# Performance work log

Measured on AMD Instinct MI355X. Metric: run time of the kernel, lower is better.

Reference implementation:

```python
import jax, jax.numpy as jnp
import numpy as np

EMBED_DIM = 1024
NUM_HEADS = 16
HEAD_DIM = EMBED_DIM // NUM_HEADS


def setup_inputs() -> dict:
    key = jax.random.key(0)
    ks = jax.random.split(key, 9)
    B, S, D = 2, 2048, EMBED_DIM
    scale = 1.0 / np.sqrt(D)
    x = jax.random.normal(ks[0], (B, S, D), dtype=jnp.float32)
    Wq = jax.random.normal(ks[1], (D, D), dtype=jnp.float32) * scale
    Wk = jax.random.normal(ks[2], (D, D), dtype=jnp.float32) * scale
    Wv = jax.random.normal(ks[3], (D, D), dtype=jnp.float32) * scale
    Wo = jax.random.normal(ks[4], (D, D), dtype=jnp.float32) * scale
    bq = jnp.zeros((D,), jnp.float32)
    bk = jnp.zeros((D,), jnp.float32)
    bv = jnp.zeros((D,), jnp.float32)
    bo = jnp.zeros((D,), jnp.float32)
    return {"x": x, "Wq": Wq, "bq": bq, "Wk": Wk, "bk": bk,
            "Wv": Wv, "bv": bv, "Wo": Wo, "bo": bo}


def reference(x, Wq, bq, Wk, bk, Wv, bv, Wo, bo):
    B, S, D = x.shape
    H, Dh = NUM_HEADS, HEAD_DIM
    # QKV projections -> [B, H, S, Dh]
    q = (x @ Wq + bq).reshape(B, S, H, Dh).transpose(0, 2, 1, 3)
    k = (x @ Wk + bk).reshape(B, S, H, Dh).transpose(0, 2, 1, 3)
    v = (x @ Wv + bv).reshape(B, S, H, Dh).transpose(0, 2, 1, 3)
    # scores [B, H, S, S], scaled by sqrt(head_dim)
    scores = jnp.einsum('bhqd,bhkd->bhqk', q, k) / jnp.sqrt(jnp.float32(Dh))
    attn = jax.nn.softmax(scores, axis=-1)
    out = jnp.einsum('bhqk,bhkd->bhqd', attn, v)  # [B, H, S, Dh]
    out = out.transpose(0, 2, 1, 3).reshape(B, S, D)
    return out @ Wo + bo
```

## Files before the change

### kernel.cpp

```cpp
#include <hip/hip_runtime.h>
#include <hip/hip_bf16.h>

typedef short bf16x8 __attribute__((ext_vector_type(8)));
typedef float f32x4 __attribute__((ext_vector_type(4)));
typedef unsigned uint2v __attribute__((ext_vector_type(2)));

#define MFMA16(a, b, c) __builtin_amdgcn_mfma_f32_16x16x32_bf16((a), (b), (c), 0, 0, 0)

#if __has_builtin(__builtin_amdgcn_exp2f)
#define EXP2(x) __builtin_amdgcn_exp2f(x)
#else
#define EXP2(x) exp2f(x)
#endif

static constexpr int B_ = 2, S_ = 2048, D_ = 1024, H_ = 16, DH = 64;
static constexpr int M_ = B_ * S_;
static constexpr int K_ = D_;
static constexpr float kQS = 0.18033688011112042f;

static __device__ __forceinline__ ushort f2bf(float f) {
    __hip_bfloat16 h = __float2bfloat16(f);
    return *reinterpret_cast<ushort*>(&h);
}

static __device__ __forceinline__ void gload16(const ushort* g, ushort* l) {
    __builtin_amdgcn_global_load_lds((const __attribute__((address_space(1))) void*)g,
                                     (__attribute__((address_space(3))) void*)l, 16, 0, 0);
}

static __device__ __forceinline__ unsigned pkbf(float lo, float hi) {
    return __builtin_amdgcn_perm(__builtin_bit_cast(unsigned, hi),
                                 __builtin_bit_cast(unsigned, lo), 0x07060302u);
}

__global__ __launch_bounds__(256) void prep5(const float* __restrict__ x,
                                             const float* __restrict__ W0,
                                             const float* __restrict__ W1,
                                             const float* __restrict__ W2,
                                             const float* __restrict__ W3,
                                             ushort* __restrict__ xb,
                                             ushort* __restrict__ T0,
                                             ushort* __restrict__ T1,
                                             ushort* __restrict__ T2,
                                             ushort* __restrict__ T3) {
    int z = blockIdx.z;
    int tx = threadIdx.x, ty = threadIdx.y;
    int t = ty * 32 + tx;
    if (z == 4) {
        int blk = blockIdx.y * 32 + blockIdx.x;
#pragma unroll
        for (int k = 0; k < 4; k++) {
            int i = blk * 1024 + k * 256 + t;
            float4 v = reinterpret_cast<const float4*>(x)[i];
            ushort4 o;
            o.x = f2bf(v.x); o.y = f2bf(v.y); o.z = f2bf(v.z); o.w = f2bf(v.w);
            reinterpret_cast<ushort4*>(xb)[i] = o;
        }
        return;
    }
    __shared__ float tile[32][33];
    const float* W = (z == 0) ? W0 : (z == 1) ? W1 : (z == 2) ? W2 : W3;
    ushort* T = (z == 0) ? T0 : (z == 1) ? T1 : (z == 2) ? T2 : T3;
    float sc = (z == 0) ? kQS : 1.0f;
    int bx = blockIdx.x, by = blockIdx.y;
#pragma unroll
    for (int i = 0; i < 4; i++)
        tile[ty + i * 8][tx] = W[(by * 32 + ty + i * 8) * D_ + bx * 32 + tx];
    __syncthreads();
#pragma unroll
    for (int i = 0; i < 4; i++)
        T[(bx * 32 + ty + i * 8) * K_ + by * 32 + tx] = f2bf(tile[tx][ty + i * 8] * sc);
}

template <int MODE, int TN>
__global__ __launch_bounds__(256, 3) void gemm128(const ushort* __restrict__ A,
                                                  const ushort* __restrict__ Wt,
                                                  const float* __restrict__ bias_q,
                                                  const float* __restrict__ bias_k,
                                                  const float* __restrict__ bias_v,
                                                  ushort* __restrict__ Qb,
                                                  ushort* __restrict__ Kb,
                                                  ushort* __restrict__ Vtb,
                                                  float* __restrict__ outf) {
    constexpr int NJ = TN / 32;
    __shared__ __align__(16) ushort As[128 * 32];
    __shared__ __align__(16) ushort Bs[TN * 32];

    int m0 = blockIdx.x * 128;
    int n0 = blockIdx.y * TN;
    int t = threadIdx.x;
    int lane = t & 63, w = t >> 6;
    int ln = lane & 15, lq = lane >> 4;
    int wm = (w >> 1) * 64, wn = (w & 1) * (TN / 2);

    int c0 = t, c1 = t + 256;
    const ushort* Ag0 = A + (size_t)(m0 + (c0 >> 2)) * K_ + (c0 & 3) * 8;
    const ushort* Ag1 = A + (size_t)(m0 + (c1 >> 2)) * K_ + (c1 & 3) * 8;
    const ushort* Bg0 = Wt + (size_t)(n0 + (c0 >> 2)) * K_ + (c0 & 3) * 8;
    const ushort* Bg1 = Wt + (size_t)(n0 + (c1 >> 2)) * K_ + (c1 & 3) * 8;
    ushort* Al0 = As + c0 * 8;
    ushort* Al1 = As + c1 * 8;
    ushort* Bl0 = Bs + c0 * 8;
    ushort* Bl1 = Bs + c1 * 8;

    const bool swp = (MODE == 1) || (n0 < 2048);

    f32x4 acc[4][NJ];
#pragma unroll
    for (int i = 0; i < 4; i++)
#pragma unroll
        for (int j = 0; j < NJ; j++) acc[i][j] = f32x4{0.f, 0.f, 0.f, 0.f};

    if (swp) {
        for (int k0 = 0; k0 < K_; k0 += 32) {
            gload16(Ag0 + k0, Al0);
            gload16(Ag1 + k0, Al1);
            gload16(Bg0 + k0, Bl0);
            if (TN == 128) gload16(Bg1 + k0, Bl1);
            __syncthreads();
            bf16x8 af[4], bfr[NJ];
#pragma unroll
            for (int i = 0; i < 4; i++)
                af[i] = *reinterpret_cast<const bf16x8*>(As + (wm + i * 16 + ln) * 32 + lq * 8);
#pragma unroll
            for (int j = 0; j < NJ; j++)
                bfr[j] = *reinterpret_cast<const bf16x8*>(Bs + (wn + j * 16 + ln) * 32 + lq * 8);
#pragma unroll
            for (int i = 0; i < 4; i++)
#pragma unroll
                for (int j = 0; j < NJ; j++)
                    acc[i][j] = MFMA16(bfr[j], af[i], acc[i][j]);
            __syncthreads();
        }
    } else {
        for (int k0 = 0; k0 < K_; k0 += 32) {
            gload16(Ag0 + k0, Al0);
            gload16(Ag1 + k0, Al1);
            gload16(Bg0 + k0, Bl0);
            if (TN == 128) gload16(Bg1 + k0, Bl1);
            __syncthreads();
            bf16x8 af[4], bfr[NJ];
#pragma unroll
            for (int i = 0; i < 4; i++)
                af[i] = *reinterpret_cast<const bf16x8*>(As + (wm + i * 16 + ln) * 32 + lq * 8);
#pragma unroll
            for (int j = 0; j < NJ; j++)
                bfr[j] = *reinterpret_cast<const bf16x8*>(Bs + (wn + j * 16 + ln) * 32 + lq * 8);
#pragma unroll
            for (int i = 0; i < 4; i++)
#pragma unroll
                for (int j = 0; j < NJ; j++)
                    acc[i][j] = MFMA16(af[i], bfr[j], acc[i][j]);
            __syncthreads();
        }
    }

    if (MODE == 1) {
#pragma unroll
        for (int j = 0; j < NJ; j++) {
            int nb = n0 + wn + j * 16 + lq * 4;
            float4 bv4 = *reinterpret_cast<const float4*>(bias_q + nb);
#pragma unroll
            for (int i = 0; i < 4; i++) {
                int m = m0 + wm + i * 16 + ln;
                float4 o;
                o.x = acc[i][j][0] + bv4.x;
                o.y = acc[i][j][1] + bv4.y;
                o.z = acc[i][j][2] + bv4.z;
                o.w = acc[i][j][3] + bv4.w;
                *reinterpret_cast<float4*>(outf + (size_t)m * D_ + nb) = o;
            }
        }
    } else if (n0 < 2048) {
        int which = n0 >> 10;
        const float* bp = which ? bias_k : bias_q;
        ushort* dst = which ? Kb : Qb;
        float bsc = which ? 1.0f : kQS;
#pragma unroll
        for (int j = 0; j < NJ; j++) {
            int nb = ((n0 + wn + j * 16) & 1023) + lq * 4;
            int h = nb >> 6, dhb = nb & 63;
            float4 bv4 = *reinterpret_cast<const float4*>(bp + nb);
            bv4.x *= bsc; bv4.y *= bsc; bv4.z *= bsc; bv4.w *= bsc;
#pragma unroll
            for (int i = 0; i < 4; i++) {
                int m = m0 + wm + i * 16 + ln;
                int b = m >> 11, s = m & 2047;
                ushort4 o4;
                o4.x = f2bf(acc[i][j][0] + bv4.x);
                o4.y = f2bf(acc[i][j][1] + bv4.y);
                o4.z = f2bf(acc[i][j][2] + bv4.z);
                o4.w = f2bf(acc[i][j][3] + bv4.w);
                *reinterpret_cast<ushort4*>(dst + (((size_t)(b * H_ + h) * S_) + s) * DH + dhb) = o4;
            }
        }
    } else {
#pragma unroll
        for (int j = 0; j < NJ; j++) {
            int n = n0 + wn + j * 16 + ln;
            int nn = n & 1023, h = nn >> 6, dh = nn & 63;
            float bv = bias_v[nn];
#pragma unroll
            for (int i = 0; i < 4; i++) {
                int m = m0 + wm + i * 16 + lq * 4;
                int b = m >> 11, s0 = m & 2047;
                ushort4 o4;
                o4.x = f2bf(acc[i][j][0] + bv);
                o4.y = f2bf(acc[i][j][1] + bv);
                o4.z = f2bf(acc[i][j][2] + bv);
                o4.w = f2bf(acc[i][j][3] + bv);
                *reinterpret_cast<ushort4*>(Vtb + (((size_t)(b * H_ + h) * DH) + dh) * S_ + s0) = o4;
            }
        }
    }
}

__global__ __launch_bounds__(256) void attn64t(const ushort* __restrict__ Q,
                                               const ushort* __restrict__ K,
                                               const ushort* __restrict__ Vt,
                                               ushort* __restrict__ O) {
    __shared__ __align__(16) ushort Kl[512 * 8];
    __shared__ __align__(16) ushort Vl[512 * 8];
    __shared__ __align__(16) ushort Pl[4][16 * 72];

    int bid = blockIdx.x;
    int qb = bid & 31;
    int bh = bid >> 5;
    int t = threadIdx.x;
    int lane = t & 63, w = t >> 6;
    int ln = lane & 15, lq = lane >> 4;
    int qt = qb * 4 + w;

    const ushort* Qp = Q + (size_t)bh * S_ * DH;
    const ushort* Kp = K + (size_t)bh * S_ * DH;
    const ushort* Vp = Vt + (size_t)bh * DH * S_;

    bf16x8 qf0 = *reinterpret_cast<const bf16x8*>(Qp + (qt * 16 + ln) * DH + lq * 8);
    bf16x8 qf1 = *reinterpret_cast<const bf16x8*>(Qp + (qt * 16 + ln) * DH + 32 + lq * 8);

    bf16x8 ones;
#pragma unroll
    for (int j = 0; j < 8; j++) ones[j] = (short)0x3F80;

    int c0 = t, c1 = t + 256;
    const ushort* Kg0 = Kp + (size_t)(c0 & 63) * DH + (c0 >> 6) * 8;
    const ushort* Kg1 = Kp + (size_t)(c1 & 63) * DH + (c1 >> 6) * 8;
    const ushort* Vg0 = Vp + (size_t)(c0 & 63) * S_ + (c0 >> 6) * 8;
    const ushort* Vg1 = Vp + (size_t)(c1 & 63) * S_ + (c1 >> 6) * 8;
    ushort* Kl0 = Kl + c0 * 8;
    ushort* Kl1 = Kl + c1 * 8;
    ushort* Vl0 = Vl + c0 * 8;
    ushort* Vl1 = Vl + c1 * 8;

    f32x4 o_acc[4];
    f32x4 l_acc = {0.f, 0.f, 0.f, 0.f};
#pragma unroll
    for (int nt = 0; nt < 4; nt++) o_acc[nt] = f32x4{0.f, 0.f, 0.f, 0.f};

    for (int kt = 0; kt < S_ / 64; kt++) {
        int kb = kt * 64;
        gload16(Kg0 + (size_t)kb * DH, Kl0);
        gload16(Kg1 + (size_t)kb * DH, Kl1);
        gload16(Vg0 + kb, Vl0);
        gload16(Vg1 + kb, Vl1);
        __syncthreads();

        f32x4 sc[4];
#pragma unroll
        for (int nt = 0; nt < 4; nt++) {
            bf16x8 kf0 = *reinterpret_cast<const bf16x8*>(Kl + (lq * 64 + nt * 16 + ln) * 8);
            bf16x8 kf1 = *reinterpret_cast<const bf16x8*>(Kl + ((4 + lq) * 64 + nt * 16 + ln) * 8);
            f32x4 c = {0.f, 0.f, 0.f, 0.f};
            c = MFMA16(kf0, qf0, c);
            c = MFMA16(kf1, qf1, c);
            sc[nt] = c;
        }
#pragma unroll
        for (int nt = 0; nt < 4; nt++) {
            float p0 = EXP2(sc[nt][0]);
            float p1 = EXP2(sc[nt][1]);
            float p2 = EXP2(sc[nt][2]);
            float p3 = EXP2(sc[nt][3]);
            uint2v pk;
            pk.x = pkbf(p0, p1);
            pk.y = pkbf(p2, p3);
            *reinterpret_cast<uint2v*>(&Pl[w][ln * 72 + nt * 16 + lq * 4]) = pk;
        }
        bf16x8 pf0 = *reinterpret_cast<const bf16x8*>(&Pl[w][ln * 72 + lq * 8]);
        bf16x8 pf1 = *reinterpret_cast<const bf16x8*>(&Pl[w][ln * 72 + 32 + lq * 8]);
        l_acc = MFMA16(pf0, ones, l_acc);
        l_acc = MFMA16(pf1, ones, l_acc);
#pragma unroll
        for (int nt = 0; nt < 4; nt++) {
            bf16x8 vf0 = *reinterpret_cast<const bf16x8*>(Vl + (lq * 64 + nt * 16 + ln) * 8);
            bf16x8 vf1 = *reinterpret_cast<const bf16x8*>(Vl + ((4 + lq) * 64 + nt * 16 + ln) * 8);
            o_acc[nt] = MFMA16(pf0, vf0, o_acc[nt]);
            o_acc[nt] = MFMA16(pf1, vf1, o_acc[nt]);
        }
        __syncthreads();
    }

    float linv[4];
#pragma unroll
    for (int r = 0; r < 4; r++) linv[r] = 1.0f / l_acc[r];
    int b = bh >> 4, h = bh & 15;
#pragma unroll
    for (int nt = 0; nt < 4; nt++)
#pragma unroll
        for (int r = 0; r < 4; r++) {
            int s = qt * 16 + lq * 4 + r;
            O[((b * S_ + s) * H_ + h) * DH + nt * 16 + ln] =
                f2bf(o_acc[nt][r] * linv[r]);
        }
}

extern "C" void kernel_launch(void* const* d_in, const int* in_sizes, int n_in,
                              void* d_out, int out_size, void* d_ws, size_t ws_size,
                              hipStream_t stream) {
    const float* x  = (const float*)d_in[0];
    const float* Wq = (const float*)d_in[1];
    const float* bq = (const float*)d_in[2];
    const float* Wk = (const float*)d_in[3];
    const float* bk = (const float*)d_in[4];
    const float* Wv = (const float*)d_in[5];
    const float* bv = (const float*)d_in[6];
    const float* Wo = (const float*)d_in[7];
    const float* bo = (const float*)d_in[8];
    float* out = (float*)d_out;

    char* ws = (char*)d_ws;
    const size_t MB = 1024 * 1024;
    ushort* wtq = (ushort*)(ws + 0 * MB);
    ushort* wtk = (ushort*)(ws + 2 * MB);
    ushort* wtv = (ushort*)(ws + 4 * MB);
    ushort* wto = (ushort*)(ws + 6 * MB);
    ushort* xb  = (ushort*)(ws + 8 * MB);
    ushort* Qb  = (ushort*)(ws + 16 * MB);
    ushort* Kb  = (ushort*)(ws + 24 * MB);
    ushort* Vtb = (ushort*)(ws + 32 * MB);
    ushort* AO  = (ushort*)(ws + 40 * MB);

    prep5<<<dim3(32, 32, 5), dim3(32, 8), 0, stream>>>(
        x, Wq, Wk, Wv, Wo, xb, wtq, wtk, wtv, wto);

    gemm128<0, 128><<<dim3(M_ / 128, 3072 / 128), 256, 0, stream>>>(
        xb, wtq, bq, bk, bv, Qb, Kb, Vtb, nullptr);

    attn64t<<<32 * 32, 256, 0, stream>>>(Qb, Kb, Vtb, AO);

    gemm128<1, 64><<<dim3(M_ / 128, D_ / 64), 256, 0, stream>>>(
        AO, wto, bo, nullptr, nullptr, nullptr, nullptr, nullptr, out);
}
```

Measured before the change: 207.1 us.

## Split attention keys in two halves with 32-row query tiles per wave and combine

The attention kernel now gives each wave two 16-row query tiles, so every K/V tile loaded into LDS feeds twice as many MFMAs. The key dimension is split into two halves across blocks, keeping the grid at 1024 blocks. Each half writes a normalized partial output plus its softmax row sums, and a new combine kernel merges them by weighted sum. This adds an extra kernel, extra global traffic for the partial outputs, and a second bf16 rounding step in exchange for better K/V reuse.

```diff
diff --git a/kernel.cpp b/kernel.cpp
--- a/kernel.cpp
+++ b/kernel.cpp
@@ -21,6 +21,11 @@
 static __device__ __forceinline__ ushort f2bf(float f) {
     __hip_bfloat16 h = __float2bfloat16(f);
     return *reinterpret_cast<ushort*>(&h);
+}
+static __device__ __forceinline__ float bf2f(ushort u) {
+    __hip_bfloat16 h;
+    *reinterpret_cast<ushort*>(&h) = u;
+    return __bfloat162float(h);
 }
 
 static __device__ __forceinline__ void gload16(const ushort* g, ushort* l) {
@@ -215,28 +220,37 @@
     }
 }
 
-__global__ __launch_bounds__(256) void attn64t(const ushort* __restrict__ Q,
-                                               const ushort* __restrict__ K,
-                                               const ushort* __restrict__ Vt,
-                                               ushort* __restrict__ O) {
+__global__ __launch_bounds__(256, 4) void attn128s(const ushort* __restrict__ Q,
+                                                   const ushort* __restrict__ K,
+                                                   const ushort* __restrict__ Vt,
+                                                   ushort* __restrict__ O1,
+                                                   ushort* __restrict__ O2,
+                                                   float* __restrict__ L) {
     __shared__ __align__(16) ushort Kl[512 * 8];
     __shared__ __align__(16) ushort Vl[512 * 8];
-    __shared__ __align__(16) ushort Pl[4][16 * 72];
+    __shared__ __align__(16) ushort Pl[4][2][16 * 72];
 
     int bid = blockIdx.x;
-    int qb = bid & 31;
-    int bh = bid >> 5;
+    int half = bid >> 9;
+    int rem = bid & 511;
+    int qb = rem & 15;
+    int bh = rem >> 4;
     int t = threadIdx.x;
     int lane = t & 63, w = t >> 6;
     int ln = lane & 15, lq = lane >> 4;
-    int qt = qb * 4 + w;
+    int q0 = qb * 128 + w * 32;
 
     const ushort* Qp = Q + (size_t)bh * S_ * DH;
-    const ushort* Kp = K + (size_t)bh * S_ * DH;
-    const ushort* Vp = Vt + (size_t)bh * DH * S_;
-
-    bf16x8 qf0 = *reinterpret_cast<const bf16x8*>(Qp + (qt * 16 + ln) * DH + lq * 8);
-    bf16x8 qf1 = *reinterpret_cast<const bf16x8*>(Qp + (qt * 16 + ln) * DH + 32 + lq * 8);
+    const ushort* Kp = K + (size_t)bh * S_ * DH + (size_t)half * 1024 * DH;
+    const ushort* Vp = Vt + (size_t)bh * DH * S_ + (size_t)half * 1024;
+
+    bf16x8 qf[2][2];
+#pragma unroll
+    for (int tl = 0; tl < 2; tl++) {
+        const ushort* qp = Qp + (q0 + tl * 16 + ln) * DH + lq * 8;
+        qf[tl][0] = *reinterpret_cast<const bf16x8*>(qp);
+        qf[tl][1] = *reinterpret_cast<const bf16x8*>(qp + 32);
+    }
 
     bf16x8 ones;
 #pragma unroll
@@ -252,12 +266,16 @@
     ushort* Vl0 = Vl + c0 * 8;
     ushort* Vl1 = Vl + c1 * 8;
 
-    f32x4 o_acc[4];
-    f32x4 l_acc = {0.f, 0.f, 0.f, 0.f};
-#pragma unroll
-    for (int nt = 0; nt < 4; nt++) o_acc[nt] = f32x4{0.f, 0.f, 0.f, 0.f};
-
-    for (int kt = 0; kt < S_ / 64; kt++) {
+    f32x4 o_acc[2][4];
+    f32x4 l_acc[2];
+#pragma unroll
+    for (int tl = 0; tl < 2; tl++) {
+        l_acc[tl] = f32x4{0.f, 0.f, 0.f, 0.f};
+#pragma unroll
+        for (int nt = 0; nt < 4; nt++) o_acc[tl][nt] = f32x4{0.f, 0.f, 0.f, 0.f};
+    }
+
+    for (int kt = 0; kt < 16; kt++) {
         int kb = kt * 64;
         gload16(Kg0 + (size_t)kb * DH, Kl0);
         gload16(Kg1 + (size_t)kb * DH, Kl1);
@@ -265,53 +283,105 @@
         gload16(Vg1 + kb, Vl1);
         __syncthreads();
 
-        f32x4 sc[4];
+        f32x4 sc[2][4];
 #pragma unroll
         for (int nt = 0; nt < 4; nt++) {
             bf16x8 kf0 = *reinterpret_cast<const bf16x8*>(Kl + (lq * 64 + nt * 16 + ln) * 8);
             bf16x8 kf1 = *reinterpret_cast<const bf16x8*>(Kl + ((4 + lq) * 64 + nt * 16 + ln) * 8);
-            f32x4 c = {0.f, 0.f, 0.f, 0.f};
-            c = MFMA16(kf0, qf0, c);
-            c = MFMA16(kf1, qf1, c);
-            sc[nt] = c;
-        }
-#pragma unroll
-        for (int nt = 0; nt < 4; nt++) {
-            float p0 = EXP2(sc[nt][0]);
-            float p1 = EXP2(sc[nt][1]);
-            float p2 = EXP2(sc[nt][2]);
-            float p3 = EXP2(sc[nt][3]);
-            uint2v pk;
-            pk.x = pkbf(p0, p1);
-            pk.y = pkbf(p2, p3);
-            *reinterpret_cast<uint2v*>(&Pl[w][ln * 72 + nt * 16 + lq * 4]) = pk;
-        }
-        bf16x8 pf0 = *reinterpret_cast<const bf16x8*>(&Pl[w][ln * 72 + lq * 8]);
-        bf16x8 pf1 = *reinterpret_cast<const bf16x8*>(&Pl[w][ln * 72 + 32 + lq * 8]);
-        l_acc = MFMA16(pf0, ones, l_acc);
-        l_acc = MFMA16(pf1, ones, l_acc);
+#pragma unroll
+            for (int tl = 0; tl < 2; tl++) {
+                f32x4 c = {0.f, 0.f, 0.f, 0.f};
+                c = MFMA16(kf0, qf[tl][0], c);
+                c = MFMA16(kf1, qf[tl][1], c);
+                sc[tl][nt] = c;
+            }
+        }
+#pragma unroll
+        for (int tl = 0; tl < 2; tl++)
+#pragma unroll
+            for (int nt = 0; nt < 4; nt++) {
+                float p0 = EXP2(sc[tl][nt][0]);
+                float p1 = EXP2(sc[tl][nt][1]);
+                float p2 = EXP2(sc[tl][nt][2]);
+                float p3 = EXP2(sc[tl][nt][3]);
+                uint2v pk;
+                pk.x = pkbf(p0, p1);
+                pk.y = pkbf(p2, p3);
+                *reinterpret_cast<uint2v*>(&Pl[w][tl][ln * 72 + nt * 16 + lq * 4]) = pk;
+            }
+        bf16x8 pf[2][2];
+#pragma unroll
+        for (int tl = 0; tl < 2; tl++) {
+            pf[tl][0] = *reinterpret_cast<const bf16x8*>(&Pl[w][tl][ln * 72 + lq * 8]);
+            pf[tl][1] = *reinterpret_cast<const bf16x8*>(&Pl[w][tl][ln * 72 + 32 + lq * 8]);
+            l_acc[tl] = MFMA16(pf[tl][0], ones, l_acc[tl]);
+            l_acc[tl] = MFMA16(pf[tl][1], ones, l_acc[tl]);
+        }
 #pragma unroll
         for (int nt = 0; nt < 4; nt++) {
             bf16x8 vf0 = *reinterpret_cast<const bf16x8*>(Vl + (lq * 64 + nt * 16 + ln) * 8);
             bf16x8 vf1 = *reinterpret_cast<const bf16x8*>(Vl + ((4 + lq) * 64 + nt * 16 + ln) * 8);
-            o_acc[nt] = MFMA16(pf0, vf0, o_acc[nt]);
-            o_acc[nt] = MFMA16(pf1, vf1, o_acc[nt]);
+#pragma unroll
+            for (int tl = 0; tl < 2; tl++) {
+                o_acc[tl][nt] = MFMA16(pf[tl][0], vf0, o_acc[tl][nt]);
+                o_acc[tl][nt] = MFMA16(pf[tl][1], vf1, o_acc[tl][nt]);
+            }
         }
         __syncthreads();
     }
 
-    float linv[4];
-#pragma unroll
-    for (int r = 0; r < 4; r++) linv[r] = 1.0f / l_acc[r];
+    ushort* Op = half ? O2 : O1;
+    float* Lp = L + ((size_t)half * 32 + bh) * S_;
     int b = bh >> 4, h = bh & 15;
 #pragma unroll
-    for (int nt = 0; nt < 4; nt++)
+    for (int tl = 0; tl < 2; tl++) {
+        float linv[4];
 #pragma unroll
         for (int r = 0; r < 4; r++) {
-            int s = qt * 16 + lq * 4 + r;
-            O[((b * S_ + s) * H_ + h) * DH + nt * 16 + ln] =
-                f2bf(o_acc[nt][r] * linv[r]);
-        }
+            linv[r] = 1.0f / l_acc[tl][r];
+            if (ln == 0) Lp[q0 + tl * 16 + lq * 4 + r] = l_acc[tl][r];
+        }
+#pragma unroll
+        for (int nt = 0; nt < 4; nt++)
+#pragma unroll
+            for (int r = 0; r < 4; r++) {
+                int s = q0 + tl * 16 + lq * 4 + r;
+                Op[((b * S_ + s) * H_ + h) * DH + nt * 16 + ln] =
+                    f2bf(o_acc[tl][nt][r] * linv[r]);
+            }
+    }
+}
+
+__global__ __launch_bounds__(256) void attn_comb(const ushort* __restrict__ O1,
+                                                 const ushort* __restrict__ O2,
+                                                 const float* __restrict__ L,
+                                                 ushort* __restrict__ AO) {
+    int i = blockIdx.x * 256 + threadIdx.x;
+    int row = i >> 7;
+    int col = (i & 127) * 8;
+    int h = col >> 6;
+    int b = row >> 11, s = row & 2047;
+    int bh = b * 16 + h;
+    float l1 = L[(size_t)bh * S_ + s];
+    float l2 = L[((size_t)32 + bh) * S_ + s];
+    float inv = 1.0f / (l1 + l2);
+    float w1 = l1 * inv, w2 = l2 * inv;
+    size_t off = (size_t)row * D_ + col;
+    ushort4 a0 = reinterpret_cast<const ushort4*>(O1 + off)[0];
+    ushort4 a1 = reinterpret_cast<const ushort4*>(O1 + off)[1];
+    ushort4 b0 = reinterpret_cast<const ushort4*>(O2 + off)[0];
+    ushort4 b1 = reinterpret_cast<const ushort4*>(O2 + off)[1];
+    ushort4 o0, o1v;
+    o0.x = f2bf(w1 * bf2f(a0.x) + w2 * bf2f(b0.x));
+    o0.y = f2bf(w1 * bf2f(a0.y) + w2 * bf2f(b0.y));
+    o0.z = f2bf(w1 * bf2f(a0.z) + w2 * bf2f(b0.z));
+    o0.w = f2bf(w1 * bf2f(a0.w) + w2 * bf2f(b0.w));
+    o1v.x = f2bf(w1 * bf2f(a1.x) + w2 * bf2f(b1.x));
+    o1v.y = f2bf(w1 * bf2f(a1.y) + w2 * bf2f(b1.y));
+    o1v.z = f2bf(w1 * bf2f(a1.z) + w2 * bf2f(b1.z));
+    o1v.w = f2bf(w1 * bf2f(a1.w) + w2 * bf2f(b1.w));
+    reinterpret_cast<ushort4*>(AO + off)[0] = o0;
+    reinterpret_cast<ushort4*>(AO + off)[1] = o1v;
 }
 
 extern "C" void kernel_launch(void* const* d_in, const int* in_sizes, int n_in,
@@ -339,6 +409,9 @@
     ushort* Kb  = (ushort*)(ws + 24 * MB);
     ushort* Vtb = (ushort*)(ws + 32 * MB);
     ushort* AO  = (ushort*)(ws + 40 * MB);
+    ushort* O1  = (ushort*)(ws + 8 * MB);
+    ushort* O2  = (ushort*)(ws + 48 * MB);
+    float*  Lw  = (float*)(ws + 56 * MB);
 
     prep5<<<dim3(32, 32, 5), dim3(32, 8), 0, stream>>>(
         x, Wq, Wk, Wv, Wo, xb, wtq, wtk, wtv, wto);
@@ -346,7 +419,8 @@
     gemm128<0, 128><<<dim3(M_ / 128, 3072 / 128), 256, 0, stream>>>(
         xb, wtq, bq, bk, bv, Qb, Kb, Vtb, nullptr);
 
-    attn64t<<<32 * 32, 256, 0, stream>>>(Qb, Kb, Vtb, AO);
+    attn128s<<<1024, 256, 0, stream>>>(Qb, Kb, Vtb, O1, O2, Lw);
+    attn_comb<<<(M_ * D_ / 8) / 256, 256, 0, stream>>>(O1, O2, Lw, AO);
 
     gemm128<1, 64><<<dim3(M_ / 128, D_ / 64), 256, 0, stream>>>(
         AO, wto, bo, nullptr, nullptr, nullptr, nullptr, nullptr, out);
```

New measurement: 198.8 us. 4.0% less time.

## Split attention key tiles across waves with cross-wave output reduction

Applied to the files above, without the earlier changes.

Each wave now handles a 16-key slice of every 64-key tile for all 64 queries of the block, instead of one 16-query tile against all keys. The S^T result is reused directly as the B operand of a 16x16x16 MFMA for PV, which removes the LDS round trip for P and the ones-MFMA used for the row sum. Row sums are accumulated in registers with shuffles. Partial outputs are then reduced across waves through LDS at the end. In exchange the kernel uses more accumulator registers (64 floats of o_acc), issues more MFMAs at half K-depth, and adds an epilogue reduction with extra barriers.

```diff
diff --git a/kernel.cpp b/kernel.cpp
--- a/kernel.cpp
+++ b/kernel.cpp
@@ -2,10 +2,17 @@
 #include <hip/hip_bf16.h>
 
 typedef short bf16x8 __attribute__((ext_vector_type(8)));
+typedef short bf16x4 __attribute__((ext_vector_type(4)));
 typedef float f32x4 __attribute__((ext_vector_type(4)));
 typedef unsigned uint2v __attribute__((ext_vector_type(2)));
 
 #define MFMA16(a, b, c) __builtin_amdgcn_mfma_f32_16x16x32_bf16((a), (b), (c), 0, 0, 0)
+
+#if __has_builtin(__builtin_amdgcn_mfma_f32_16x16x16_bf16)
+#define MFMAK16(a, b, c) __builtin_amdgcn_mfma_f32_16x16x16_bf16((a), (b), (c), 0, 0, 0)
+#else
+#define MFMAK16(a, b, c) __builtin_amdgcn_mfma_f32_16x16x16bf16_1k((a), (b), (c), 0, 0, 0)
+#endif
 
 #if __has_builtin(__builtin_amdgcn_exp2f)
 #define EXP2(x) __builtin_amdgcn_exp2f(x)
@@ -215,13 +222,15 @@
     }
 }
 
-__global__ __launch_bounds__(256) void attn64t(const ushort* __restrict__ Q,
+__global__ __launch_bounds__(256) void attn_ks(const ushort* __restrict__ Q,
                                                const ushort* __restrict__ K,
                                                const ushort* __restrict__ Vt,
                                                ushort* __restrict__ O) {
-    __shared__ __align__(16) ushort Kl[512 * 8];
-    __shared__ __align__(16) ushort Vl[512 * 8];
-    __shared__ __align__(16) ushort Pl[4][16 * 72];
+    __shared__ __align__(16) ushort SM[8192 + 512];
+    ushort* Kl = SM;
+    ushort* Vl = SM + 4096;
+    float* Ored = (float*)SM;
+    float* lw = (float*)(SM + 8192);
 
     int bid = blockIdx.x;
     int qb = bid & 31;
@@ -229,18 +238,19 @@
     int t = threadIdx.x;
     int lane = t & 63, w = t >> 6;
     int ln = lane & 15, lq = lane >> 4;
-    int qt = qb * 4 + w;
+    int q0 = qb * 64;
 
     const ushort* Qp = Q + (size_t)bh * S_ * DH;
     const ushort* Kp = K + (size_t)bh * S_ * DH;
     const ushort* Vp = Vt + (size_t)bh * DH * S_;
 
-    bf16x8 qf0 = *reinterpret_cast<const bf16x8*>(Qp + (qt * 16 + ln) * DH + lq * 8);
-    bf16x8 qf1 = *reinterpret_cast<const bf16x8*>(Qp + (qt * 16 + ln) * DH + 32 + lq * 8);
-
-    bf16x8 ones;
-#pragma unroll
-    for (int j = 0; j < 8; j++) ones[j] = (short)0x3F80;
+    bf16x8 qf[4][2];
+#pragma unroll
+    for (int qt = 0; qt < 4; qt++) {
+        const ushort* qp = Qp + (q0 + qt * 16 + ln) * DH + lq * 8;
+        qf[qt][0] = *reinterpret_cast<const bf16x8*>(qp);
+        qf[qt][1] = *reinterpret_cast<const bf16x8*>(qp + 32);
+    }
 
     int c0 = t, c1 = t + 256;
     const ushort* Kg0 = Kp + (size_t)(c0 & 63) * DH + (c0 >> 6) * 8;
@@ -252,10 +262,12 @@
     ushort* Vl0 = Vl + c0 * 8;
     ushort* Vl1 = Vl + c1 * 8;
 
-    f32x4 o_acc[4];
-    f32x4 l_acc = {0.f, 0.f, 0.f, 0.f};
-#pragma unroll
-    for (int nt = 0; nt < 4; nt++) o_acc[nt] = f32x4{0.f, 0.f, 0.f, 0.f};
+    f32x4 o_acc[4][4];
+    float l_part[4] = {0.f, 0.f, 0.f, 0.f};
+#pragma unroll
+    for (int nt = 0; nt < 4; nt++)
+#pragma unroll
+        for (int qt = 0; qt < 4; qt++) o_acc[nt][qt] = f32x4{0.f, 0.f, 0.f, 0.f};
 
     for (int kt = 0; kt < S_ / 64; kt++) {
         int kb = kt * 64;
@@ -265,53 +277,74 @@
         gload16(Vg1 + kb, Vl1);
         __syncthreads();
 
-        f32x4 sc[4];
-#pragma unroll
-        for (int nt = 0; nt < 4; nt++) {
-            bf16x8 kf0 = *reinterpret_cast<const bf16x8*>(Kl + (lq * 64 + nt * 16 + ln) * 8);
-            bf16x8 kf1 = *reinterpret_cast<const bf16x8*>(Kl + ((4 + lq) * 64 + nt * 16 + ln) * 8);
+        bf16x8 kf0 = *reinterpret_cast<const bf16x8*>(Kl + (lq * 64 + w * 16 + ln) * 8);
+        bf16x8 kf1 = *reinterpret_cast<const bf16x8*>(Kl + ((4 + lq) * 64 + w * 16 + ln) * 8);
+
+        bf16x4 pfr[4];
+#pragma unroll
+        for (int qt = 0; qt < 4; qt++) {
             f32x4 c = {0.f, 0.f, 0.f, 0.f};
-            c = MFMA16(kf0, qf0, c);
-            c = MFMA16(kf1, qf1, c);
-            sc[nt] = c;
-        }
-#pragma unroll
-        for (int nt = 0; nt < 4; nt++) {
-            float p0 = EXP2(sc[nt][0]);
-            float p1 = EXP2(sc[nt][1]);
-            float p2 = EXP2(sc[nt][2]);
-            float p3 = EXP2(sc[nt][3]);
+            c = MFMA16(kf0, qf[qt][0], c);
+            c = MFMA16(kf1, qf[qt][1], c);
+            float p0 = EXP2(c[0]);
+            float p1 = EXP2(c[1]);
+            float p2 = EXP2(c[2]);
+            float p3 = EXP2(c[3]);
+            l_part[qt] += (p0 + p1) + (p2 + p3);
             uint2v pk;
             pk.x = pkbf(p0, p1);
             pk.y = pkbf(p2, p3);
-            *reinterpret_cast<uint2v*>(&Pl[w][ln * 72 + nt * 16 + lq * 4]) = pk;
-        }
-        bf16x8 pf0 = *reinterpret_cast<const bf16x8*>(&Pl[w][ln * 72 + lq * 8]);
-        bf16x8 pf1 = *reinterpret_cast<const bf16x8*>(&Pl[w][ln * 72 + 32 + lq * 8]);
-        l_acc = MFMA16(pf0, ones, l_acc);
-        l_acc = MFMA16(pf1, ones, l_acc);
+            pfr[qt] = __builtin_bit_cast(bf16x4, pk);
+        }
 #pragma unroll
         for (int nt = 0; nt < 4; nt++) {
-            bf16x8 vf0 = *reinterpret_cast<const bf16x8*>(Vl + (lq * 64 + nt * 16 + ln) * 8);
-            bf16x8 vf1 = *reinterpret_cast<const bf16x8*>(Vl + ((4 + lq) * 64 + nt * 16 + ln) * 8);
-            o_acc[nt] = MFMA16(pf0, vf0, o_acc[nt]);
-            o_acc[nt] = MFMA16(pf1, vf1, o_acc[nt]);
+            bf16x4 vf = *reinterpret_cast<const bf16x4*>(
+                Vl + ((w * 2 + (lq >> 1)) * 64 + nt * 16 + ln) * 8 + (lq & 1) * 4);
+#pragma unroll
+            for (int qt = 0; qt < 4; qt++)
+                o_acc[nt][qt] = MFMAK16(vf, pfr[qt], o_acc[nt][qt]);
         }
         __syncthreads();
     }
 
-    float linv[4];
-#pragma unroll
-    for (int r = 0; r < 4; r++) linv[r] = 1.0f / l_acc[r];
+#pragma unroll
+    for (int qt = 0; qt < 4; qt++) {
+        l_part[qt] += __shfl_xor(l_part[qt], 16, 64);
+        l_part[qt] += __shfl_xor(l_part[qt], 32, 64);
+    }
+    if (lq == 0) {
+#pragma unroll
+        for (int qt = 0; qt < 4; qt++) lw[(w * 4 + qt) * 16 + ln] = l_part[qt];
+    }
+
     int b = bh >> 4, h = bh & 15;
-#pragma unroll
-    for (int nt = 0; nt < 4; nt++)
-#pragma unroll
-        for (int r = 0; r < 4; r++) {
-            int s = qt * 16 + lq * 4 + r;
-            O[((b * S_ + s) * H_ + h) * DH + nt * 16 + ln] =
-                f2bf(o_acc[nt][r] * linv[r]);
-        }
+    float linv = 0.f;
+#pragma unroll
+    for (int nt = 0; nt < 4; nt++) {
+        __syncthreads();
+#pragma unroll
+        for (int qt = 0; qt < 4; qt++)
+            *reinterpret_cast<f32x4*>(Ored + w * 1024 + qt * 256 + lane * 4) = o_acc[nt][qt];
+        __syncthreads();
+        f32x4 s = {0.f, 0.f, 0.f, 0.f};
+#pragma unroll
+        for (int wv = 0; wv < 4; wv++) {
+            f32x4 p = *reinterpret_cast<const f32x4*>(Ored + wv * 1024 + w * 256 + lane * 4);
+            s[0] += p[0]; s[1] += p[1]; s[2] += p[2]; s[3] += p[3];
+        }
+        if (nt == 0) {
+            float L = lw[(0 * 4 + w) * 16 + ln] + lw[(1 * 4 + w) * 16 + ln] +
+                      lw[(2 * 4 + w) * 16 + ln] + lw[(3 * 4 + w) * 16 + ln];
+            linv = 1.0f / L;
+        }
+        ushort4 o4;
+        o4.x = f2bf(s[0] * linv);
+        o4.y = f2bf(s[1] * linv);
+        o4.z = f2bf(s[2] * linv);
+        o4.w = f2bf(s[3] * linv);
+        int sq = q0 + w * 16 + ln;
+        *reinterpret_cast<ushort4*>(O + ((size_t)(b * S_ + sq) * H_ + h) * DH + nt * 16 + lq * 4) = o4;
+    }
 }
 
 extern "C" void kernel_launch(void* const* d_in, const int* in_sizes, int n_in,
@@ -346,7 +379,7 @@
     gemm128<0, 128><<<dim3(M_ / 128, 3072 / 128), 256, 0, stream>>>(
         xb, wtq, bq, bk, bv, Qb, Kb, Vtb, nullptr);
 
-    attn64t<<<32 * 32, 256, 0, stream>>>(Qb, Kb, Vtb, AO);
+    attn_ks<<<32 * 32, 256, 0, stream>>>(Qb, Kb, Vtb, AO);
 
     gemm128<1, 64><<<dim3(M_ / 128, D_ / 64), 256, 0, stream>>>(
         AO, wto, bo, nullptr, nullptr, nullptr, nullptr, nullptr, out);
```

Result: slower. 238.6 us (+15.2%).
